# Optimization experiments

Hardware: AMD Instinct MI355X
Metric: run time of the kernel (lower is better)

Reference implementation:

```python
import jax, jax.numpy as jnp
import numpy as np

D_MODEL = 1024
N_HEADS = 16
HEAD_DIM = D_MODEL // N_HEADS


def setup_inputs() -> dict:
    key = jax.random.key(0)
    ks = jax.random.split(key, 9)
    B, T, S, D = 4, 2048, 512, D_MODEL
    sc = 1.0 / np.sqrt(D)
    return {
        "x": jax.random.normal(ks[0], (B, T, D), dtype=jnp.float32),
        "context": jax.random.normal(ks[1], (B, S, D), dtype=jnp.float32),
        "context_mask": jnp.ones((B, S), dtype=bool),
        "Wq": jax.random.normal(ks[2], (D, D), dtype=jnp.float32) * sc,
        "bq": jnp.zeros((D,), dtype=jnp.float32),
        "Wkv": jax.random.normal(ks[3], (D, 2 * D), dtype=jnp.float32) * sc,
        "bkv": jnp.zeros((2 * D,), dtype=jnp.float32),
        "Wp": jax.random.normal(ks[4], (D, D), dtype=jnp.float32) * sc,
        "bp": jnp.zeros((D,), dtype=jnp.float32),
    }


def reference(x, context, context_mask, Wq, bq, Wkv, bkv, Wp, bp):
    B, T, D = x.shape
    S = context.shape[1]
    H, Hd = N_HEADS, HEAD_DIM
    # projections
    q = (x @ Wq + bq).reshape(B, T, H, Hd).transpose(0, 2, 1, 3)          # [B,H,T,Hd]
    kv = (context @ Wkv + bkv).reshape(B, S, 2, H, Hd)
    k = kv[:, :, 0].transpose(0, 2, 1, 3)                                  # [B,H,S,Hd]
    v = kv[:, :, 1].transpose(0, 2, 1, 3)                                  # [B,H,S,Hd]
    # scaled dot-product attention with context mask
    scores = jnp.einsum("bhtd,bhsd->bhts", q, k) / np.sqrt(Hd)            # [B,H,T,S]
    neg_inf = jnp.finfo(scores.dtype).min
    scores = jnp.where(context_mask[:, None, None, :], scores, neg_inf)
    attn = jax.nn.softmax(scores, axis=-1)
    # dropout is identity in eval mode (p applied only in training)
    out = jnp.einsum("bhts,bhsd->bthd", attn, v).reshape(B, T, D)
    return out @ Wp + bp
```

## Files before the change

kernel.cpp:

```cpp
#include <hip/hip_runtime.h>

typedef __bf16 bf16x8 __attribute__((ext_vector_type(8)));
typedef float  f32x4  __attribute__((ext_vector_type(4)));
typedef float  f32x16 __attribute__((ext_vector_type(16)));
typedef unsigned int u32x2 __attribute__((ext_vector_type(2)));

#define MFMA(a, b, c)   __builtin_amdgcn_mfma_f32_16x16x32_bf16((a), (b), (c), 0, 0, 0)
#define MFMA32(a, b, c) __builtin_amdgcn_mfma_f32_32x32x16_bf16((a), (b), (c), 0, 0, 0)

#define GLL(g, l) __builtin_amdgcn_global_load_lds(                                  \
    (const __attribute__((address_space(1))) void*)(g),                              \
    (__attribute__((address_space(3))) void*)(l), 16, 0, 0)

#define BB 4
#define TT 2048
#define SS 512
#define DM 1024
#define NH 16
#define HD 64

__device__ __forceinline__ unsigned short f2bh(float f) {
    __bf16 h = (__bf16)f;
    union { __bf16 h; unsigned short u; } v; v.h = h;
    return v.u;
}

__device__ __forceinline__ unsigned int pk2(float a, float b) {
    return (unsigned int)f2bh(a) | ((unsigned int)f2bh(b) << 16);
}

__device__ __forceinline__ void pl32swap(unsigned int& a, unsigned int& b) {
    u32x2 r = __builtin_amdgcn_permlane32_swap(a, b, false, false);
    a = r[0]; b = r[1];
}

__device__ __forceinline__ void tcast_tile(const float* __restrict__ in,
                                           unsigned short* __restrict__ out,
                                           int K, int N, int n0, int k0,
                                           float (*tile)[33], int tid) {
    int tx = tid & 31, ty = tid >> 5;
#pragma unroll
    for (int r = 0; r < 32; r += 8)
        tile[ty + r][tx] = in[(k0 + ty + r) * N + n0 + tx];
    __syncthreads();
    int r2 = tid >> 3, cg = (tid & 7) * 4;
    ushort4 o;
    o.x = f2bh(tile[cg + 0][r2]);
    o.y = f2bh(tile[cg + 1][r2]);
    o.z = f2bh(tile[cg + 2][r2]);
    o.w = f2bh(tile[cg + 3][r2]);
    *(ushort4*)&out[(n0 + r2) * K + k0 + cg] = o;
}

__global__ __launch_bounds__(256)
void prep(const float4* __restrict__ x, const float4* __restrict__ ctx,
          const unsigned int* __restrict__ mw,
          const float* __restrict__ Wq, const float* __restrict__ Wkv,
          const float* __restrict__ Wp,
          ushort4* __restrict__ Xbf, ushort4* __restrict__ Cbf,
          unsigned short* __restrict__ WqT, unsigned short* __restrict__ WkvT,
          unsigned short* __restrict__ WpT, float* __restrict__ mbias) {
    __shared__ float tile[32][33];
    __shared__ int flags[2];
    const int bid = blockIdx.x, tid = threadIdx.x;
    if (bid < 8192) {
        int i = bid * 256 + tid;
        float4 v = x[i];
        ushort4 o; o.x = f2bh(v.x); o.y = f2bh(v.y); o.z = f2bh(v.z); o.w = f2bh(v.w);
        Xbf[i] = o;
    } else if (bid < 10240) {
        int i = (bid - 8192) * 256 + tid;
        float4 v = ctx[i];
        ushort4 o; o.x = f2bh(v.x); o.y = f2bh(v.y); o.z = f2bh(v.z); o.w = f2bh(v.w);
        Cbf[i] = o;
    } else if (bid < 11264) {
        int loc = bid - 10240;
        tcast_tile(Wq, WqT, DM, DM, (loc & 31) * 32, (loc >> 5) * 32, tile, tid);
    } else if (bid < 13312) {
        int loc = bid - 11264;
        tcast_tile(Wkv, WkvT, DM, 2 * DM, (loc & 63) * 32, (loc >> 6) * 32, tile, tid);
    } else if (bid < 14336) {
        int loc = bid - 13312;
        tcast_tile(Wp, WpT, DM, DM, (loc & 31) * 32, (loc >> 5) * 32, tile, tid);
    } else {
        if (tid == 0) { flags[0] = 1; flags[1] = 1; }
        __syncthreads();
        int okI = 1, okF = 1;
        for (int i = tid; i < 512; i += 256) {
            unsigned int w = mw[i];
            if (w > 1u) okI = 0;
            if (w != 0u && w != 0x3f800000u) okF = 0;
        }
        if (!okI) atomicAnd(&flags[0], 0);
        if (!okF) atomicAnd(&flags[1], 0);
        __syncthreads();
        bool wordLayout = (flags[0] != 0) || (flags[1] != 0);
        const unsigned char* mb = (const unsigned char*)mw;
        for (int s = tid; s < BB * SS; s += 256) {
            bool on = wordLayout ? (mw[s] != 0u) : (mb[s] != 0);
            mbias[s] = on ? 0.0f : -1e38f;
        }
    }
}

__device__ __forceinline__ void gemm_core(
    const unsigned short* __restrict__ A, const unsigned short* __restrict__ Bt,
    int K, int m0, int n0, unsigned short* As, unsigned short* Bs,
    f32x4 (*acc)[4]) {
    const int tid = threadIdx.x;
    const int l = tid & 63;
    const int quad = l >> 4, col = l & 15;
    const int w = tid >> 6;
    const int wm = (w & 1) * 64, wn = (w >> 1) * 64;
    const int arow = tid >> 3;
    const int apiece = (tid & 7) ^ (arow & 7);
    const unsigned short* Ab = A + (size_t)(m0 + arow) * K + apiece * 8;
    const unsigned short* Bb = Bt + (size_t)(n0 + arow) * K + apiece * 8;

    for (int k0 = 0; k0 < K; k0 += 64) {
        __syncthreads();
#pragma unroll
        for (int g = 0; g < 4; ++g)
            GLL(Ab + k0 + g * 32 * K, &As[g * 2048 + tid * 8]);
#pragma unroll
        for (int g = 0; g < 4; ++g)
            GLL(Bb + k0 + g * 32 * K, &Bs[g * 2048 + tid * 8]);
        __syncthreads();
#pragma unroll
        for (int k32 = 0; k32 < 2; ++k32) {
            bf16x8 af[4], bfr[4];
#pragma unroll
            for (int i = 0; i < 4; i++) {
                int rr = wm + i * 16 + col;
                af[i] = *(const bf16x8*)&As[rr * 64 + (((k32 * 4 + quad) ^ (rr & 7)) * 8)];
            }
#pragma unroll
            for (int j = 0; j < 4; j++) {
                int rr = wn + j * 16 + col;
                bfr[j] = *(const bf16x8*)&Bs[rr * 64 + (((k32 * 4 + quad) ^ (rr & 7)) * 8)];
            }
#pragma unroll
            for (int i = 0; i < 4; i++)
#pragma unroll
                for (int j = 0; j < 4; j++) acc[i][j] = MFMA(af[i], bfr[j], acc[i][j]);
        }
    }
}

__global__ __launch_bounds__(256, 3)
void gemm_qkv(const unsigned short* __restrict__ Xbf, const unsigned short* __restrict__ WqT,
              const float* __restrict__ bq, unsigned short* __restrict__ Qb,
              const unsigned short* __restrict__ Cbf, const unsigned short* __restrict__ WkvT,
              const float* __restrict__ bkv, unsigned short* __restrict__ Kb,
              unsigned short* __restrict__ Vtb) {
    __shared__ __align__(16) unsigned short As[128 * 64];
    __shared__ __align__(16) unsigned short Bs[128 * 64];
    const int tid = threadIdx.x;
    const int l = tid & 63;
    const int quad = l >> 4, col = l & 15;
    const int w = tid >> 6;
    const int wm = (w & 1) * 64, wn = (w >> 1) * 64;
    const int bid = blockIdx.x;

    const f32x4 zero = {0.f, 0.f, 0.f, 0.f};
    f32x4 acc[4][4];
#pragma unroll
    for (int i = 0; i < 4; i++)
#pragma unroll
        for (int j = 0; j < 4; j++) acc[i][j] = zero;

    if (bid < 512) {
        const int xg = bid & 7, t = bid >> 3;
        const int m0 = (xg + 8 * (t & 7)) * 128;
        const int n0 = (t >> 3) * 128;
        gemm_core(Xbf, WqT, DM, m0, n0, As, Bs, acc);
        const float QS = 0.125f * 1.4426950408889634f;
#pragma unroll
        for (int i = 0; i < 4; i++) {
#pragma unroll
            for (int j = 0; j < 4; j++) {
                int n = n0 + wn + j * 16 + col;
                int mb = m0 + wm + i * 16 + quad * 4;
                float bv = bq[n];
#pragma unroll
                for (int ii = 0; ii < 4; ii++)
                    Qb[(mb + ii) * DM + n] = f2bh((acc[i][j][ii] + bv) * QS);
            }
        }
    } else {
        const int loc = bid - 512;
        const int xg = loc & 7, t = loc >> 3;
        const int m0 = (xg + 8 * (t & 1)) * 128;
        const int n0 = (t >> 1) * 128;
        gemm_core(Cbf, WkvT, DM, m0, n0, As, Bs, acc);
#pragma unroll
        for (int i = 0; i < 4; i++) {
#pragma unroll
            for (int j = 0; j < 4; j++) {
                int n = n0 + wn + j * 16 + col;
                int mb = m0 + wm + i * 16 + quad * 4;
                float bv = bkv[n];
                if (n < 1024) {
                    int h = n >> 6, d = n & 63;
#pragma unroll
                    for (int ii = 0; ii < 4; ii++) {
                        int m = mb + ii; int b = m >> 9, s = m & 511;
                        Kb[(((b * NH + h) * SS) + s) * HD + d] = f2bh(acc[i][j][ii] + bv);
                    }
                } else {
                    int q = n - 1024; int h = q >> 6, d = q & 63;
#pragma unroll
                    for (int ii = 0; ii < 4; ii++) {
                        int m = mb + ii; int b = m >> 9, s = m & 511;
                        Vtb[(((b * NH + h) * HD) + d) * SS + s] = f2bh(acc[i][j][ii] + bv);
                    }
                }
            }
        }
    }
}

__global__ __launch_bounds__(256, 3)
void gemm_out(const unsigned short* __restrict__ Ob, const unsigned short* __restrict__ WpT,
              const float* __restrict__ bp, float* __restrict__ out) {
    __shared__ __align__(16) unsigned short As[128 * 64];
    __shared__ __align__(16) unsigned short Bs[128 * 64];
    const int tid = threadIdx.x;
    const int l = tid & 63;
    const int quad = l >> 4, col = l & 15;
    const int w = tid >> 6;
    const int wm = (w & 1) * 64, wn = (w >> 1) * 64;
    const int bid = blockIdx.x;
    const int xg = bid & 7, t = bid >> 3;
    const int m0 = (xg + 8 * (t & 7)) * 128;
    const int n0 = (t >> 3) * 128;

    const f32x4 zero = {0.f, 0.f, 0.f, 0.f};
    f32x4 acc[4][4];
#pragma unroll
    for (int i = 0; i < 4; i++)
#pragma unroll
        for (int j = 0; j < 4; j++) acc[i][j] = zero;

    gemm_core(Ob, WpT, DM, m0, n0, As, Bs, acc);

#pragma unroll
    for (int i = 0; i < 4; i++) {
#pragma unroll
        for (int j = 0; j < 4; j++) {
            int n = n0 + wn + j * 16 + col;
            int mb = m0 + wm + i * 16 + quad * 4;
            float bv = bp[n];
#pragma unroll
            for (int ii = 0; ii < 4; ii++)
                out[(mb + ii) * DM + n] = acc[i][j][ii] + bv;
        }
    }
}

__global__ __launch_bounds__(512, 4)
void flash_attn(const unsigned short* __restrict__ Q, const unsigned short* __restrict__ Kb,
                const unsigned short* __restrict__ Vt, const float* __restrict__ mbias,
                unsigned short* __restrict__ O) {
    const int bid = blockIdx.x;
    const int xg = bid & 7, tq = bid >> 3;
    const int tb = tq & 7;
    const int bh = xg + 8 * (tq >> 3);
    const int b = bh >> 4;
    const int tid = threadIdx.x;
    const int w = tid >> 6, l = tid & 63;
    const int lq = l & 31, hi = l >> 5;

    __shared__ __align__(16) unsigned short Ks[2][64 * 64];
    __shared__ __align__(16) unsigned short Vs[2][64 * 64];
    __shared__ float biasS[SS];

    const unsigned short* Kh = Kb + bh * SS * HD;
    const unsigned short* Vh = Vt + bh * HD * SS;

    float bval = mbias[b * SS + tid];
    biasS[tid] = bval;
    const int allon = __syncthreads_and(bval == 0.0f);

    const int rowbase = b * TT + tb * 256 + w * 32;
    const int hd0 = (bh & 15) * HD;

    const unsigned short* qrow = Q + (size_t)(rowbase + lq) * DM + hd0;
    bf16x8 qf[4];
#pragma unroll
    for (int ch = 0; ch < 4; ++ch)
        qf[ch] = *(const bf16x8*)(qrow + ch * 16 + hi * 8);

    const int sr = tid >> 3, sp = tid & 7;
    const int spk = ((sp ^ (sr & 7)) * 8);
    const int kgo = sr * HD + spk;
    const int vgo = sr * SS + spk;

    GLL(Kh + kgo, &Ks[0][tid * 8]);
    GLL(Vh + vgo, &Vs[0][tid * 8]);

    const f32x16 zero16 = {0.f,0.f,0.f,0.f,0.f,0.f,0.f,0.f,
                           0.f,0.f,0.f,0.f,0.f,0.f,0.f,0.f};
    f32x16 oacc0 = zero16, oacc1 = zero16;
    float lsum = 0.f;

    for (int it = 0; it < SS / 64; ++it) {
        const int s0 = it * 64;
        const int buf = it & 1;
        __syncthreads();
        if (it + 1 < SS / 64) {
            GLL(Kh + (s0 + 64) * HD + kgo, &Ks[buf ^ 1][tid * 8]);
            GLL(Vh + (s0 + 64) + vgo, &Vs[buf ^ 1][tid * 8]);
        }

        f32x16 cs0 = zero16, cs1 = zero16;
        __builtin_amdgcn_s_setprio(1);
#pragma unroll
        for (int ch = 0; ch < 4; ++ch) {
            const int p0 = ((2 * ch + hi) ^ (lq & 7)) * 8;
            bf16x8 k0 = *(const bf16x8*)&Ks[buf][lq * 64 + p0];
            bf16x8 k1 = *(const bf16x8*)&Ks[buf][(lq + 32) * 64 + p0];
            cs0 = MFMA32(k0, qf[ch], cs0);
            cs1 = MFMA32(k1, qf[ch], cs1);
        }
        __builtin_amdgcn_s_setprio(0);

        bf16x8 pfrag[4];
#pragma unroll
        for (int sg = 0; sg < 2; ++sg) {
            float pr[16];
#pragma unroll
            for (int r = 0; r < 16; ++r) {
                float sc = (sg == 0) ? cs0[r] : cs1[r];
                if (!allon)
                    sc += biasS[s0 + 32 * sg + ((r & 3) + 8 * (r >> 2) + 4 * hi)];
                pr[r] = exp2f(sc);
                lsum += pr[r];
            }
            unsigned int wd0 = pk2(pr[0], pr[1]),  wd1 = pk2(pr[2], pr[3]);
            unsigned int wd2 = pk2(pr[4], pr[5]),  wd3 = pk2(pr[6], pr[7]);
            unsigned int wd4 = pk2(pr[8], pr[9]),  wd5 = pk2(pr[10], pr[11]);
            unsigned int wd6 = pk2(pr[12], pr[13]), wd7 = pk2(pr[14], pr[15]);
            pl32swap(wd0, wd2); pl32swap(wd1, wd3);
            pl32swap(wd4, wd6); pl32swap(wd5, wd7);
            union { unsigned int u[4]; bf16x8 v; } f0, f1;
            f0.u[0] = wd0; f0.u[1] = wd1; f0.u[2] = wd2; f0.u[3] = wd3;
            f1.u[0] = wd4; f1.u[1] = wd5; f1.u[2] = wd6; f1.u[3] = wd7;
            pfrag[2 * sg + 0] = f0.v;
            pfrag[2 * sg + 1] = f1.v;
        }

        __builtin_amdgcn_s_setprio(1);
#pragma unroll
        for (int win = 0; win < 4; ++win) {
            const int pv0 = ((2 * win + hi) ^ (lq & 7)) * 8;
            bf16x8 v0 = *(const bf16x8*)&Vs[buf][lq * 64 + pv0];
            bf16x8 v1 = *(const bf16x8*)&Vs[buf][(lq + 32) * 64 + pv0];
            oacc0 = MFMA32(pfrag[win], v0, oacc0);
            oacc1 = MFMA32(pfrag[win], v1, oacc1);
        }
        __builtin_amdgcn_s_setprio(0);
    }

    lsum += __shfl_xor(lsum, 32);
    float inv = 1.0f / lsum;
    union { float f; int i; } cv; cv.f = inv;
#pragma unroll
    for (int r = 0; r < 16; ++r) {
        const int qloc = (r & 3) + 8 * (r >> 2) + 4 * hi;
        union { int i; float f; } rv;
        rv.i = __builtin_amdgcn_ds_bpermute(4 * qloc, cv.i);
        const float iq = rv.f;
        unsigned short* orow = O + (size_t)(rowbase + qloc) * DM + hd0 + lq;
        orow[0]  = f2bh(oacc0[r] * iq);
        orow[32] = f2bh(oacc1[r] * iq);
    }
}

extern "C" void kernel_launch(void* const* d_in, const int* in_sizes, int n_in,
                              void* d_out, int out_size, void* d_ws, size_t ws_size,
                              hipStream_t stream) {
    const float* x    = (const float*)d_in[0];
    const float* ctx  = (const float*)d_in[1];
    const void*  cmsk = d_in[2];
    const float* Wq   = (const float*)d_in[3];
    const float* bq   = (const float*)d_in[4];
    const float* Wkv  = (const float*)d_in[5];
    const float* bkv  = (const float*)d_in[6];
    const float* Wp   = (const float*)d_in[7];
    const float* bp   = (const float*)d_in[8];
    float* out = (float*)d_out;

    char* ws = (char*)d_ws;
    size_t off = 0;
    auto alloc = [&](size_t bytes) -> void* {
        void* p = ws + off;
        off += (bytes + 255) & ~(size_t)255;
        return p;
    };
    const size_t NX = (size_t)BB * TT * DM;
    const size_t NC = (size_t)BB * SS * DM;
    unsigned short* Xbf  = (unsigned short*)alloc(NX * 2);
    unsigned short* Cbf  = (unsigned short*)alloc(NC * 2);
    unsigned short* WqT  = (unsigned short*)alloc((size_t)DM * DM * 2);
    unsigned short* WkvT = (unsigned short*)alloc((size_t)DM * 2 * DM * 2);
    unsigned short* WpT  = (unsigned short*)alloc((size_t)DM * DM * 2);
    unsigned short* Qb   = (unsigned short*)alloc(NX * 2);
    unsigned short* Kbf  = (unsigned short*)alloc(NC * 2);
    unsigned short* Vtb  = (unsigned short*)alloc(NC * 2);
    unsigned short* Ob   = (unsigned short*)alloc(NX * 2);
    float* mbias         = (float*)alloc((size_t)BB * SS * 4);

    prep<<<14337, 256, 0, stream>>>((const float4*)x, (const float4*)ctx,
                                    (const unsigned int*)cmsk, Wq, Wkv, Wp,
                                    (ushort4*)Xbf, (ushort4*)Cbf,
                                    WqT, WkvT, WpT, mbias);

    gemm_qkv<<<768, 256, 0, stream>>>(Xbf, WqT, bq, Qb, Cbf, WkvT, bkv, Kbf, Vtb);

    flash_attn<<<BB * NH * (TT / 256), 512, 0, stream>>>(Qb, Kbf, Vtb, mbias, Ob);

    gemm_out<<<512, 256, 0, stream>>>(Ob, WpT, bp, out);
}
```

Measured before the change: 200.4 us.

## Halve flash-attention block size and interleave QK/PV per 32-key half

The attention kernel now uses 256-thread blocks covering 128 query rows, with twice as many blocks, and each thread issues two async loads per K/V tile. The per-tile loop is restructured to compute scores, softmax and PV for one 32-key half at a time, which cuts live registers (one score accumulator instead of two). exp2f is replaced with raw v_exp_f32 inline asm, and the row-sum accumulation becomes a tree sum. The aim is lower register pressure and better occupancy and latency hiding. In exchange, K/V tiles are reloaded by more blocks, and the raw exp skips exp2f's edge-case handling.

```diff
diff --git a/kernel.cpp b/kernel.cpp
--- a/kernel.cpp
+++ b/kernel.cpp
@@ -32,6 +32,12 @@
 __device__ __forceinline__ void pl32swap(unsigned int& a, unsigned int& b) {
     u32x2 r = __builtin_amdgcn_permlane32_swap(a, b, false, false);
     a = r[0]; b = r[1];
+}
+
+__device__ __forceinline__ float fexp2(float x) {
+    float e;
+    asm("v_exp_f32 %0, %1" : "=v"(e) : "v"(x));
+    return e;
 }
 
 __device__ __forceinline__ void tcast_tile(const float* __restrict__ in,
@@ -258,14 +264,14 @@
     }
 }
 
-__global__ __launch_bounds__(512, 4)
+__global__ __launch_bounds__(256, 4)
 void flash_attn(const unsigned short* __restrict__ Q, const unsigned short* __restrict__ Kb,
                 const unsigned short* __restrict__ Vt, const float* __restrict__ mbias,
                 unsigned short* __restrict__ O) {
     const int bid = blockIdx.x;
     const int xg = bid & 7, tq = bid >> 3;
-    const int tb = tq & 7;
-    const int bh = xg + 8 * (tq >> 3);
+    const int tb = tq & 15;
+    const int bh = xg + 8 * (tq >> 4);
     const int b = bh >> 4;
     const int tid = threadIdx.x;
     const int w = tid >> 6, l = tid & 63;
@@ -278,11 +284,12 @@
     const unsigned short* Kh = Kb + bh * SS * HD;
     const unsigned short* Vh = Vt + bh * HD * SS;
 
-    float bval = mbias[b * SS + tid];
-    biasS[tid] = bval;
-    const int allon = __syncthreads_and(bval == 0.0f);
-
-    const int rowbase = b * TT + tb * 256 + w * 32;
+    float bv0 = mbias[b * SS + tid];
+    float bv1 = mbias[b * SS + 256 + tid];
+    biasS[tid] = bv0; biasS[tid + 256] = bv1;
+    const int allon = __syncthreads_and((bv0 == 0.0f) && (bv1 == 0.0f));
+
+    const int rowbase = b * TT + tb * 128 + w * 32;
     const int hd0 = (bh & 15) * HD;
 
     const unsigned short* qrow = Q + (size_t)(rowbase + lq) * DM + hd0;
@@ -291,13 +298,17 @@
     for (int ch = 0; ch < 4; ++ch)
         qf[ch] = *(const bf16x8*)(qrow + ch * 16 + hi * 8);
 
-    const int sr = tid >> 3, sp = tid & 7;
-    const int spk = ((sp ^ (sr & 7)) * 8);
-    const int kgo = sr * HD + spk;
-    const int vgo = sr * SS + spk;
-
-    GLL(Kh + kgo, &Ks[0][tid * 8]);
-    GLL(Vh + vgo, &Vs[0][tid * 8]);
+    const int r0 = tid >> 3, sp = tid & 7;
+    const int r1 = r0 + 32;
+    const int kgo0 = r0 * HD + ((sp ^ (r0 & 7)) * 8);
+    const int kgo1 = r1 * HD + ((sp ^ (r1 & 7)) * 8);
+    const int vgo0 = r0 * SS + ((sp ^ (r0 & 7)) * 8);
+    const int vgo1 = r1 * SS + ((sp ^ (r1 & 7)) * 8);
+
+    GLL(Kh + kgo0, &Ks[0][tid * 8]);
+    GLL(Kh + kgo1, &Ks[0][2048 + tid * 8]);
+    GLL(Vh + vgo0, &Vs[0][tid * 8]);
+    GLL(Vh + vgo1, &Vs[0][2048 + tid * 8]);
 
     const f32x16 zero16 = {0.f,0.f,0.f,0.f,0.f,0.f,0.f,0.f,
                            0.f,0.f,0.f,0.f,0.f,0.f,0.f,0.f};
@@ -309,57 +320,58 @@
         const int buf = it & 1;
         __syncthreads();
         if (it + 1 < SS / 64) {
-            GLL(Kh + (s0 + 64) * HD + kgo, &Ks[buf ^ 1][tid * 8]);
-            GLL(Vh + (s0 + 64) + vgo, &Vs[buf ^ 1][tid * 8]);
-        }
-
-        f32x16 cs0 = zero16, cs1 = zero16;
-        __builtin_amdgcn_s_setprio(1);
-#pragma unroll
-        for (int ch = 0; ch < 4; ++ch) {
-            const int p0 = ((2 * ch + hi) ^ (lq & 7)) * 8;
-            bf16x8 k0 = *(const bf16x8*)&Ks[buf][lq * 64 + p0];
-            bf16x8 k1 = *(const bf16x8*)&Ks[buf][(lq + 32) * 64 + p0];
-            cs0 = MFMA32(k0, qf[ch], cs0);
-            cs1 = MFMA32(k1, qf[ch], cs1);
-        }
-        __builtin_amdgcn_s_setprio(0);
-
-        bf16x8 pfrag[4];
-#pragma unroll
-        for (int sg = 0; sg < 2; ++sg) {
+            GLL(Kh + (s0 + 64) * HD + kgo0, &Ks[buf ^ 1][tid * 8]);
+            GLL(Kh + (s0 + 64) * HD + kgo1, &Ks[buf ^ 1][2048 + tid * 8]);
+            GLL(Vh + (s0 + 64) + vgo0, &Vs[buf ^ 1][tid * 8]);
+            GLL(Vh + (s0 + 64) + vgo1, &Vs[buf ^ 1][2048 + tid * 8]);
+        }
+
+#pragma unroll
+        for (int t = 0; t < 2; ++t) {
+            const int rk = lq + 32 * t;
+            f32x16 cs = zero16;
+            __builtin_amdgcn_s_setprio(1);
+#pragma unroll
+            for (int ch = 0; ch < 4; ++ch) {
+                bf16x8 kf = *(const bf16x8*)&Ks[buf][rk * 64 + (((2 * ch + hi) ^ (lq & 7)) * 8)];
+                cs = MFMA32(kf, qf[ch], cs);
+            }
+            __builtin_amdgcn_s_setprio(0);
+
             float pr[16];
 #pragma unroll
             for (int r = 0; r < 16; ++r) {
-                float sc = (sg == 0) ? cs0[r] : cs1[r];
+                float sc = cs[r];
                 if (!allon)
-                    sc += biasS[s0 + 32 * sg + ((r & 3) + 8 * (r >> 2) + 4 * hi)];
-                pr[r] = exp2f(sc);
-                lsum += pr[r];
-            }
-            unsigned int wd0 = pk2(pr[0], pr[1]),  wd1 = pk2(pr[2], pr[3]);
-            unsigned int wd2 = pk2(pr[4], pr[5]),  wd3 = pk2(pr[6], pr[7]);
-            unsigned int wd4 = pk2(pr[8], pr[9]),  wd5 = pk2(pr[10], pr[11]);
+                    sc += biasS[s0 + 32 * t + ((r & 3) + 8 * (r >> 2) + 4 * hi)];
+                pr[r] = fexp2(sc);
+            }
+            lsum += ((pr[0] + pr[1]) + (pr[2] + pr[3])) + ((pr[4] + pr[5]) + (pr[6] + pr[7]))
+                  + ((pr[8] + pr[9]) + (pr[10] + pr[11])) + ((pr[12] + pr[13]) + (pr[14] + pr[15]));
+            unsigned int wd0 = pk2(pr[0], pr[1]),   wd1 = pk2(pr[2], pr[3]);
+            unsigned int wd2 = pk2(pr[4], pr[5]),   wd3 = pk2(pr[6], pr[7]);
+            unsigned int wd4 = pk2(pr[8], pr[9]),   wd5 = pk2(pr[10], pr[11]);
             unsigned int wd6 = pk2(pr[12], pr[13]), wd7 = pk2(pr[14], pr[15]);
             pl32swap(wd0, wd2); pl32swap(wd1, wd3);
             pl32swap(wd4, wd6); pl32swap(wd5, wd7);
             union { unsigned int u[4]; bf16x8 v; } f0, f1;
             f0.u[0] = wd0; f0.u[1] = wd1; f0.u[2] = wd2; f0.u[3] = wd3;
             f1.u[0] = wd4; f1.u[1] = wd5; f1.u[2] = wd6; f1.u[3] = wd7;
-            pfrag[2 * sg + 0] = f0.v;
-            pfrag[2 * sg + 1] = f1.v;
-        }
-
-        __builtin_amdgcn_s_setprio(1);
-#pragma unroll
-        for (int win = 0; win < 4; ++win) {
-            const int pv0 = ((2 * win + hi) ^ (lq & 7)) * 8;
-            bf16x8 v0 = *(const bf16x8*)&Vs[buf][lq * 64 + pv0];
-            bf16x8 v1 = *(const bf16x8*)&Vs[buf][(lq + 32) * 64 + pv0];
-            oacc0 = MFMA32(pfrag[win], v0, oacc0);
-            oacc1 = MFMA32(pfrag[win], v1, oacc1);
-        }
-        __builtin_amdgcn_s_setprio(0);
+            bf16x8 pfrag[2];
+            pfrag[0] = f0.v;
+            pfrag[1] = f1.v;
+
+            __builtin_amdgcn_s_setprio(1);
+#pragma unroll
+            for (int win = 0; win < 2; ++win) {
+                const int p = 4 * t + 2 * win + hi;
+                bf16x8 v0 = *(const bf16x8*)&Vs[buf][lq * 64 + ((p ^ (lq & 7)) * 8)];
+                bf16x8 v1 = *(const bf16x8*)&Vs[buf][(lq + 32) * 64 + ((p ^ (lq & 7)) * 8)];
+                oacc0 = MFMA32(pfrag[win], v0, oacc0);
+                oacc1 = MFMA32(pfrag[win], v1, oacc1);
+            }
+            __builtin_amdgcn_s_setprio(0);
+        }
     }
 
     lsum += __shfl_xor(lsum, 32);
@@ -418,7 +430,7 @@
 
     gemm_qkv<<<768, 256, 0, stream>>>(Xbf, WqT, bq, Qb, Cbf, WkvT, bkv, Kbf, Vtb);
 
-    flash_attn<<<BB * NH * (TT / 256), 512, 0, stream>>>(Qb, Kbf, Vtb, mbias, Ob);
+    flash_attn<<<BB * NH * (TT / 128), 256, 0, stream>>>(Qb, Kbf, Vtb, mbias, Ob);
 
     gemm_out<<<512, 256, 0, stream>>>(Ob, WpT, bp, out);
 }
```

New measurement: 195.1 us. -2.6%, faster.
